# Optimization experiments

Hardware: AMD Instinct MI355X
Metric: run time of the kernel (lower is better)

## Reference

```python
import jax, jax.numpy as jnp
import numpy as np

D_MODEL = 256; D_FC = 1024; N_LEVELS = 4; N_HEADS = 8; N_POINTS = 4
D_HEAD = D_MODEL // N_HEADS
SPATIAL = np.array([[100, 100], [50, 50], [25, 25], [13, 13]], dtype=np.int64)
S_TOTAL = int((SPATIAL[:, 0] * SPATIAL[:, 1]).sum())  # 13294
BATCH = 2


def setup_inputs() -> dict:
    key = jax.random.key(0)
    ks = jax.random.split(key, 16)

    def lin(k, fi, fo):
        s = 1.0 / np.sqrt(fi)
        kw, kb = jax.random.split(k)
        W = jax.random.uniform(kw, (fi, fo), jnp.float32, -s, s)
        b = jax.random.uniform(kb, (fo,), jnp.float32, -s, s)
        return W, b

    W_off, b_off = lin(ks[0], D_MODEL, N_HEADS * N_LEVELS * N_POINTS * 2)
    W_attn, b_attn = lin(ks[1], D_MODEL, N_HEADS * N_LEVELS * N_POINTS)
    W_val, b_val = lin(ks[2], D_MODEL, D_MODEL)
    W_out, b_out = lin(ks[3], D_MODEL, D_MODEL)
    W1, b1 = lin(ks[4], D_MODEL, D_FC)
    W2, b2 = lin(ks[5], D_FC, D_MODEL)
    src = jax.random.normal(ks[6], (BATCH, S_TOTAL, D_MODEL), jnp.float32)
    pos = jax.random.normal(ks[7], (BATCH, S_TOTAL, D_MODEL), jnp.float32)
    reference_points = jax.random.uniform(ks[8], (BATCH, S_TOTAL, N_LEVELS, 2), jnp.float32)
    level_start_index = np.concatenate([[0], np.cumsum(SPATIAL[:, 0] * SPATIAL[:, 1])[:-1]]).astype(np.int64)
    return dict(src=src, pos=pos, reference_points=reference_points,
                spatial_shapes=SPATIAL, level_start_index=level_start_index,
                W_off=W_off, b_off=b_off, W_attn=W_attn, b_attn=b_attn,
                W_val=W_val, b_val=b_val, W_out=W_out, b_out=b_out,
                ln1_g=jnp.ones(D_MODEL, jnp.float32), ln1_b=jnp.zeros(D_MODEL, jnp.float32),
                W1=W1, b1=b1, W2=W2, b2=b2,
                ln2_g=jnp.ones(D_MODEL, jnp.float32), ln2_b=jnp.zeros(D_MODEL, jnp.float32))


def layernorm(x, g, b, eps=1e-5):
    mu = x.mean(-1, keepdims=True)
    var = ((x - mu) ** 2).mean(-1, keepdims=True)
    return (x - mu) * jax.lax.rsqrt(var + eps) * g + b


def ms_deform_attn(query, value_in, ref_pts, shapes,
                   W_off, b_off, W_attn, b_attn, W_val, b_val, W_out, b_out):
    N, Lq, _ = query.shape
    value = (value_in @ W_val + b_val).reshape(N, -1, N_HEADS, D_HEAD)
    off = (query @ W_off + b_off).reshape(N, Lq, N_HEADS, N_LEVELS, N_POINTS, 2)
    attn = (query @ W_attn + b_attn).reshape(N, Lq, N_HEADS, N_LEVELS * N_POINTS)
    attn = jax.nn.softmax(attn, -1).reshape(N, Lq, N_HEADS, N_LEVELS, N_POINTS)
    # offset normalizer is (W_l, H_l) per level
    norm = jnp.array([[w, h] for (h, w) in shapes], dtype=query.dtype)
    loc = ref_pts[:, :, None, :, None, :] + off / norm[None, None, None, :, None, :]
    out = jnp.zeros((N, Lq, N_HEADS, D_HEAD), query.dtype)
    start = 0
    for l, (H_, W_) in enumerate(shapes):
        v = value[:, start:start + H_ * W_].transpose(0, 2, 1, 3)  # [N, heads, HW, d]
        start += H_ * W_
        loc_l = loc[:, :, :, l]  # [N, Lq, heads, P, 2]
        # grid_sample(align_corners=False, padding_mode='zeros'): pixel = loc*size - 0.5
        px = loc_l[..., 0] * W_ - 0.5
        py = loc_l[..., 1] * H_ - 0.5
        x0 = jnp.floor(px); y0 = jnp.floor(py)
        wx = (px - x0)[..., None]; wy = (py - y0)[..., None]
        x0i = x0.astype(jnp.int32); y0i = y0.astype(jnp.int32)

        def samp(xi, yi):
            valid = (xi >= 0) & (xi < W_) & (yi >= 0) & (yi < H_)
            idx = jnp.clip(yi, 0, H_ - 1) * W_ + jnp.clip(xi, 0, W_ - 1)  # [N,Lq,heads,P]
            idx = idx.transpose(0, 2, 1, 3).reshape(N, N_HEADS, Lq * N_POINTS, 1)
            g = jnp.take_along_axis(v, idx, axis=2)  # [N,heads,Lq*P,d]
            g = g.reshape(N, N_HEADS, Lq, N_POINTS, D_HEAD).transpose(0, 2, 1, 3, 4)
            return g * valid[..., None]

        val = (samp(x0i, y0i) * (1 - wx) * (1 - wy)
               + samp(x0i + 1, y0i) * wx * (1 - wy)
               + samp(x0i, y0i + 1) * (1 - wx) * wy
               + samp(x0i + 1, y0i + 1) * wx * wy)  # [N,Lq,heads,P,d]
        out = out + (val * attn[:, :, :, l, :, None]).sum(3)
    return out.reshape(N, Lq, D_MODEL) @ W_out + b_out


def reference(src, pos, reference_points, spatial_shapes, level_start_index,
              W_off, b_off, W_attn, b_attn, W_val, b_val, W_out, b_out,
              ln1_g, ln1_b, W1, b1, W2, b2, ln2_g, ln2_b):
    shapes = [(int(spatial_shapes[l, 0]), int(spatial_shapes[l, 1])) for l in range(N_LEVELS)]
    q = src + pos
    attn_out = ms_deform_attn(q, src, reference_points, shapes,
                              W_off, b_off, W_attn, b_attn, W_val, b_val, W_out, b_out)
    x = layernorm(src + attn_out, ln1_g, ln1_b)  # dropout is identity in eval
    ffn = jax.nn.relu(x @ W1 + b1) @ W2 + b2
    return layernorm(x + ffn, ln2_g, ln2_b)
```

## Files before the change

kernel.cpp:

```cpp
#include <hip/hip_runtime.h>
#include <hip/hip_bf16.h>

#define DM 256
#define STOT 13294
#define MTOT (2 * STOT)

using bf16 = __hip_bfloat16;
typedef __attribute__((ext_vector_type(8))) short short8;
typedef __attribute__((ext_vector_type(4))) float floatx4;

#define GLDS16(g, l) __builtin_amdgcn_global_load_lds( \
    (const __attribute__((address_space(1))) void*)(g), \
    (__attribute__((address_space(3))) void*)(l), 16, 0, 0)

__device__ __forceinline__ float bu2f(unsigned u) { return __uint_as_float(u << 16); }
__device__ __forceinline__ unsigned short f2bu(float f) {
    union { bf16 h; unsigned short u; } c; c.h = __float2bfloat16(f); return c.u;
}

__global__ void detect_dtype(const unsigned* g1, int* flag) {
    if (threadIdx.x == 0 && blockIdx.x == 0)
        *flag = (g1[0] == 0x3F800000u) ? 1 : 0;
}

struct PW { const void* W[6]; const void* B[10]; };

__global__ void prep_weights(PW a, bf16* __restrict__ WT, float* __restrict__ bf,
                             const int* __restrict__ flag) {
    const long id = (long)blockIdx.x * 256 + threadIdx.x;
    const bool f32in = (*flag != 0);
    const int sz[6]  = {65536, 65536, 32768, 65536, 262144, 262144};
    const int Ns[6]  = {256, 256, 128, 256, 1024, 256};
    const int Ksh[6] = {8, 8, 8, 8, 8, 10};
    if (id < 753664) {
        long e = id; int j = 0;
        while (e >= sz[j]) { e -= sz[j]; ++j; }
        const int n = (int)(e >> Ksh[j]);
        const int k = (int)(e & ((1 << Ksh[j]) - 1));
        const size_t src = (size_t)k * Ns[j] + n;
        float v = f32in ? ((const float*)a.W[j])[src] : __bfloat162float(((const bf16*)a.W[j])[src]);
        WT[id] = __float2bfloat16(v);
    } else if (id < 753664 + 3200) {
        long e = id - 753664; int j = 0;
        const int bsz[10] = {256, 256, 128, 256, 1024, 256, 256, 256, 256, 256};
        while (e >= bsz[j]) { e -= bsz[j]; ++j; }
        float v = f32in ? ((const float*)a.B[j])[e] : __bfloat162float(((const bf16*)a.B[j])[e]);
        bf[id - 753664] = v;
    }
}

__global__ void prep_act(const void* __restrict__ src, const void* __restrict__ pos,
                         bf16* __restrict__ sbf, bf16* __restrict__ qbf,
                         const int* __restrict__ flag) {
    const long i = ((long)blockIdx.x * 256 + threadIdx.x) * 8;
    if (i >= (long)MTOT * DM) return;
    unsigned short ps[8], pq[8];
    if (*flag) {
        const float* s = (const float*)src + i;
        const float* p = (const float*)pos + i;
        float4 a0 = *(const float4*)s, a1 = *(const float4*)(s + 4);
        float4 b0 = *(const float4*)p, b1 = *(const float4*)(p + 4);
        const float av[8] = {a0.x, a0.y, a0.z, a0.w, a1.x, a1.y, a1.z, a1.w};
        const float bv[8] = {b0.x, b0.y, b0.z, b0.w, b1.x, b1.y, b1.z, b1.w};
#pragma unroll
        for (int j = 0; j < 8; ++j) { ps[j] = f2bu(av[j]); pq[j] = f2bu(av[j] + bv[j]); }
    } else {
        const unsigned short* s = (const unsigned short*)src + i;
        const unsigned short* p = (const unsigned short*)pos + i;
        uint4 a = *(const uint4*)s, b = *(const uint4*)p;
        const unsigned* ua = (const unsigned*)&a;
        const unsigned* ub = (const unsigned*)&b;
#pragma unroll
        for (int j = 0; j < 4; ++j) {
            float a0 = bu2f(ua[j] & 0xffffu), a1 = bu2f(ua[j] >> 16);
            float b0 = bu2f(ub[j] & 0xffffu), b1 = bu2f(ub[j] >> 16);
            ps[j * 2] = f2bu(a0); ps[j * 2 + 1] = f2bu(a1);
            pq[j * 2] = f2bu(a0 + b0); pq[j * 2 + 1] = f2bu(a1 + b1);
        }
    }
    *(uint4*)((unsigned short*)sbf + i) = *(const uint4*)ps;
    *(uint4*)((unsigned short*)qbf + i) = *(const uint4*)pq;
}

template<bool RELU>
__global__ __launch_bounds__(256, 4)
void gemm_bf16(const bf16* __restrict__ A0, const bf16* __restrict__ A1, int n_a0,
               const bf16* __restrict__ WT, const float* __restrict__ bias,
               bf16* __restrict__ C0, bf16* __restrict__ C1, bf16* __restrict__ C2,
               int M, int N, int K, int ldc0) {
    __shared__ __align__(16) bf16 sh[16384];
    const int t = threadIdx.x;
    const int wave = t >> 6, lane = t & 63;
    const int bm = blockIdx.y * 128, bn = blockIdx.x * 128;
    const bf16* __restrict__ A = (bn < n_a0) ? A0 : A1;
    const int wm = (wave >> 1) * 64, wn = (wave & 1) * 64;
    const int l15 = lane & 15, quad = lane >> 4;
    const int srow = lane >> 2, sko = (lane & 3) * 8;

    floatx4 acc[4][4];
#pragma unroll
    for (int i = 0; i < 4; ++i)
#pragma unroll
        for (int j = 0; j < 4; ++j) acc[i][j] = (floatx4)0.f;

    const int nb = K >> 5;
#pragma unroll
    for (int rh = 0; rh < 2; ++rh) {
        const int rbase = rh * 64 + wave * 16;
        const int gm = min(bm + rbase + srow, M - 1);
        GLDS16(A + (size_t)gm * K + sko, &sh[rbase * 32]);
        GLDS16(WT + (size_t)(bn + rbase + srow) * K + sko, &sh[8192 + rbase * 32]);
    }
    for (int i = 0; i < nb; ++i) {
        __syncthreads();
        if (i + 1 < nb) {
            const int k0 = (i + 1) << 5;
            const int bo = ((i + 1) & 1) * 4096;
#pragma unroll
            for (int rh = 0; rh < 2; ++rh) {
                const int rbase = rh * 64 + wave * 16;
                const int gm = min(bm + rbase + srow, M - 1);
                GLDS16(A + (size_t)gm * K + k0 + sko, &sh[bo + rbase * 32]);
                GLDS16(WT + (size_t)(bn + rbase + srow) * K + k0 + sko, &sh[8192 + bo + rbase * 32]);
            }
        }
        const int bo = (i & 1) * 4096;
        short8 af[4], bfr[4];
#pragma unroll
        for (int mi = 0; mi < 4; ++mi)
            af[mi] = *(const short8*)&sh[bo + (wm + mi * 16 + l15) * 32 + quad * 8];
#pragma unroll
        for (int nj = 0; nj < 4; ++nj)
            bfr[nj] = *(const short8*)&sh[8192 + bo + (wn + nj * 16 + l15) * 32 + quad * 8];
#pragma unroll
        for (int mi = 0; mi < 4; ++mi)
#pragma unroll
            for (int nj = 0; nj < 4; ++nj)
                acc[mi][nj] = __builtin_amdgcn_mfma_f32_16x16x32_bf16(bfr[nj], af[mi], acc[mi][nj], 0, 0, 0);
    }

    bf16* C = C0; int coloff = bn, ldc = ldc0;
    if (C1 != nullptr && bn >= 256) {
        if (C2 != nullptr && bn >= 512) { C = C2; coloff = bn - 512; ldc = 128; }
        else                            { C = C1; coloff = bn - 256; ldc = 256; }
    }
    float4 bv4[4];
#pragma unroll
    for (int nj = 0; nj < 4; ++nj)
        bv4[nj] = *(const float4*)&bias[bn + wn + nj * 16 + quad * 4];
#pragma unroll
    for (int mi = 0; mi < 4; ++mi) {
        const int gm = bm + wm + mi * 16 + l15;
        if (gm >= M) continue;
#pragma unroll
        for (int nj = 0; nj < 4; ++nj) {
            const float bb[4] = {bv4[nj].x, bv4[nj].y, bv4[nj].z, bv4[nj].w};
            unsigned short pk[4];
#pragma unroll
            for (int r = 0; r < 4; ++r) {
                float v = acc[mi][nj][r] + bb[r];
                if (RELU) v = fmaxf(v, 0.f);
                pk[r] = f2bu(v);
            }
            *(uint2*)&C[(size_t)gm * ldc + coloff + wn + nj * 16 + quad * 4] = *(const uint2*)pk;
        }
    }
}

__global__ void softmax16(bf16* __restrict__ a, int total) {
    const int i = blockIdx.x * 256 + threadIdx.x;
    if (i >= total) return;
    unsigned short* p = (unsigned short*)(a + (size_t)i * 16);
    uint4 r0 = *(const uint4*)p, r1 = *(const uint4*)(p + 8);
    float w[16];
    const unsigned* u0 = (const unsigned*)&r0;
    const unsigned* u1 = (const unsigned*)&r1;
#pragma unroll
    for (int j = 0; j < 4; ++j) {
        w[j * 2] = bu2f(u0[j] & 0xffffu); w[j * 2 + 1] = bu2f(u0[j] >> 16);
        w[8 + j * 2] = bu2f(u1[j] & 0xffffu); w[8 + j * 2 + 1] = bu2f(u1[j] >> 16);
    }
    float mx = -1e30f;
#pragma unroll
    for (int j = 0; j < 16; ++j) mx = fmaxf(mx, w[j]);
    float s = 0.f;
#pragma unroll
    for (int j = 0; j < 16; ++j) { w[j] = __expf(w[j] - mx); s += w[j]; }
    const float inv = 1.f / s;
    unsigned short pk[16];
#pragma unroll
    for (int j = 0; j < 16; ++j) pk[j] = f2bu(w[j] * inv);
    *(uint4*)p = *(const uint4*)pk;
    *(uint4*)(p + 8) = *(const uint4*)(pk + 8);
}

__device__ __forceinline__ void corner(const bf16* __restrict__ base, int xi, int yi,
                                       int W_, int H_, float wgt, float* acc) {
    const bool valid = (xi >= 0) & (xi < W_) & (yi >= 0) & (yi < H_);
    const int xc = min(max(xi, 0), W_ - 1);
    const int yc = min(max(yi, 0), H_ - 1);
    const ushort4 v = *(const ushort4*)(base + (size_t)(yc * W_ + xc) * DM);
    const float m = valid ? wgt : 0.f;
    acc[0] += m * bu2f(v.x); acc[1] += m * bu2f(v.y);
    acc[2] += m * bu2f(v.z); acc[3] += m * bu2f(v.w);
}

__global__ void deform_sample(const bf16* __restrict__ value, const bf16* __restrict__ off,
                              const bf16* __restrict__ attw, const void* __restrict__ refp,
                              bf16* __restrict__ out, const int* __restrict__ flag) {
    const int t = threadIdx.x;
    const int q = blockIdx.x * 4 + (t >> 6);
    const int ln = t & 63;
    const int h = ln >> 3, dg = ln & 7;
    const int b = (q >= STOT) ? 1 : 0;

    float w[16];
    {
        const unsigned short* wp = (const unsigned short*)(attw + (size_t)q * 128 + h * 16);
        uint4 r0 = *(const uint4*)wp, r1 = *(const uint4*)(wp + 8);
        const unsigned* u0 = (const unsigned*)&r0;
        const unsigned* u1 = (const unsigned*)&r1;
#pragma unroll
        for (int j = 0; j < 4; ++j) {
            w[j * 2] = bu2f(u0[j] & 0xffffu); w[j * 2 + 1] = bu2f(u0[j] >> 16);
            w[8 + j * 2] = bu2f(u1[j] & 0xffffu); w[8 + j * 2 + 1] = bu2f(u1[j] >> 16);
        }
    }
    float of[32];
    {
        const unsigned short* op = (const unsigned short*)(off + (size_t)q * 256 + h * 32);
#pragma unroll
        for (int c = 0; c < 4; ++c) {
            uint4 r = *(const uint4*)(op + c * 8);
            const unsigned* u = (const unsigned*)&r;
#pragma unroll
            for (int j = 0; j < 4; ++j) {
                of[c * 8 + j * 2] = bu2f(u[j] & 0xffffu);
                of[c * 8 + j * 2 + 1] = bu2f(u[j] >> 16);
            }
        }
    }
    float rxy[8];
    if (*flag) {
        const float* rp = (const float*)refp + (size_t)q * 8;
        float4 r0 = *(const float4*)rp, r1 = *(const float4*)(rp + 4);
        rxy[0] = r0.x; rxy[1] = r0.y; rxy[2] = r0.z; rxy[3] = r0.w;
        rxy[4] = r1.x; rxy[5] = r1.y; rxy[6] = r1.z; rxy[7] = r1.w;
    } else {
        const unsigned short* rp = (const unsigned short*)refp + (size_t)q * 8;
        uint4 r = *(const uint4*)rp;
        const unsigned* u = (const unsigned*)&r;
#pragma unroll
        for (int j = 0; j < 4; ++j) {
            rxy[j * 2] = bu2f(u[j] & 0xffffu); rxy[j * 2 + 1] = bu2f(u[j] >> 16);
        }
    }

    const int Hs4[4] = {100, 50, 25, 13};
    const int Ls[4] = {0, 10000, 12500, 13125};
    const bf16* vb = value + (size_t)(b * STOT) * DM + h * 32 + dg * 4;

    float acc[4] = {0.f, 0.f, 0.f, 0.f};
#pragma unroll
    for (int l = 0; l < 4; ++l) {
        const int W_ = Hs4[l], H_ = Hs4[l];
        const bf16* base = vb + (size_t)Ls[l] * DM;
        const float fw = (float)W_, fh = (float)H_;
#pragma unroll
        for (int p = 0; p < 4; ++p) {
            const float px = rxy[l * 2] * fw + of[(l * 4 + p) * 2] - 0.5f;
            const float py = rxy[l * 2 + 1] * fh + of[(l * 4 + p) * 2 + 1] - 0.5f;
            const float x0f = floorf(px), y0f = floorf(py);
            const float wx = px - x0f, wy = py - y0f;
            const int x0 = (int)x0f, y0 = (int)y0f;
            const float aw = w[l * 4 + p];
            const float ex = 1.f - wx, ey = 1.f - wy;
            corner(base, x0, y0, W_, H_, ex * ey * aw, acc);
            corner(base, x0 + 1, y0, W_, H_, wx * ey * aw, acc);
            corner(base, x0, y0 + 1, W_, H_, ex * wy * aw, acc);
            corner(base, x0 + 1, y0 + 1, W_, H_, wx * wy * aw, acc);
        }
    }
    unsigned short pk[4] = {f2bu(acc[0]), f2bu(acc[1]), f2bu(acc[2]), f2bu(acc[3])};
    *(ushort4*)((unsigned short*)out + (size_t)q * 256 + h * 32 + dg * 4) = *(const ushort4*)pk;
}

__global__ __launch_bounds__(512, 1)
void out_ln1(const bf16* __restrict__ vsamp, const bf16* __restrict__ srcbf,
             const bf16* __restrict__ WoT, const float* __restrict__ bo_f,
             const float* __restrict__ g1, const float* __restrict__ be1,
             bf16* __restrict__ vx, int M) {
    __shared__ __align__(16) bf16 Bs[8 * 4096];
    const int t = threadIdx.x, wave = t >> 6, lane = t & 63;
    const int l15 = lane & 15, quad = lane >> 4;
    const int srow = lane >> 2, sko = (lane & 3) * 8;
    const int bm = blockIdx.x * 128;
    const int mrow = bm + wave * 16 + l15;
    const int mc = min(mrow, M - 1);

    short8 af[8];
#pragma unroll
    for (int kk = 0; kk < 8; ++kk)
        af[kk] = *(const short8*)(vsamp + (size_t)mc * 256 + kk * 32 + quad * 8);

    floatx4 acc[16];
#pragma unroll
    for (int i = 0; i < 16; ++i) acc[i] = (floatx4)0.f;

    for (int nc = 0; nc < 2; ++nc) {
        __syncthreads();
#pragma unroll
        for (int rr = 0; rr < 8; ++rr)
            GLDS16(WoT + (size_t)(nc * 128 + rr * 16 + srow) * 256 + wave * 32 + sko,
                   &Bs[wave * 4096 + rr * 512]);
        __syncthreads();
#pragma unroll
        for (int kk = 0; kk < 8; ++kk)
#pragma unroll
            for (int nj = 0; nj < 8; ++nj) {
                short8 bfr = *(const short8*)&Bs[kk * 4096 + (nj * 16 + l15) * 32 + quad * 8];
                acc[nc * 8 + nj] = __builtin_amdgcn_mfma_f32_16x16x32_bf16(bfr, af[kk], acc[nc * 8 + nj], 0, 0, 0);
            }
    }

    float s = 0.f;
#pragma unroll
    for (int nj = 0; nj < 16; ++nj) {
        const int n = nj * 16 + quad * 4;
        const float4 bo = *(const float4*)&bo_f[n];
        const uint2 ru = *(const uint2*)(srcbf + (size_t)mc * 256 + n);
        const float rs[4] = {bu2f(ru.x & 0xffffu), bu2f(ru.x >> 16), bu2f(ru.y & 0xffffu), bu2f(ru.y >> 16)};
        const float bb[4] = {bo.x, bo.y, bo.z, bo.w};
#pragma unroll
        for (int r = 0; r < 4; ++r) { acc[nj][r] += bb[r] + rs[r]; s += acc[nj][r]; }
    }
    s += __shfl_xor(s, 16, 64); s += __shfl_xor(s, 32, 64);
    const float mean = s * (1.f / 256.f);
    float s2 = 0.f;
#pragma unroll
    for (int nj = 0; nj < 16; ++nj)
#pragma unroll
        for (int r = 0; r < 4; ++r) { const float c = acc[nj][r] - mean; s2 += c * c; }
    s2 += __shfl_xor(s2, 16, 64); s2 += __shfl_xor(s2, 32, 64);
    const float rstd = rsqrtf(s2 * (1.f / 256.f) + 1e-5f);
    if (mrow < M) {
#pragma unroll
        for (int nj = 0; nj < 16; ++nj) {
            const int n = nj * 16 + quad * 4;
            const float4 g = *(const float4*)&g1[n];
            const float4 b = *(const float4*)&be1[n];
            const float gg[4] = {g.x, g.y, g.z, g.w}, bb[4] = {b.x, b.y, b.z, b.w};
            unsigned short pk[4];
#pragma unroll
            for (int r = 0; r < 4; ++r) pk[r] = f2bu((acc[nj][r] - mean) * rstd * gg[r] + bb[r]);
            *(uint2*)&vx[(size_t)mrow * 256 + n] = *(const uint2*)pk;
        }
    }
}

__global__ __launch_bounds__(512, 1)
void ffn_ln2(const bf16* __restrict__ vx, const bf16* __restrict__ W1T, const bf16* __restrict__ W2T,
             const float* __restrict__ b1f, const float* __restrict__ b2f,
             const float* __restrict__ g2, const float* __restrict__ be2,
             void* __restrict__ outp, const int* __restrict__ flag, int M) {
    __shared__ __align__(16) bf16 Bs1[8 * 4096];
    __shared__ __align__(16) bf16 Bs2[4 * 4096];
    __shared__ __align__(16) bf16 Hs[128 * 136];
    const int t = threadIdx.x, wave = t >> 6, lane = t & 63;
    const int l15 = lane & 15, quad = lane >> 4;
    const int srow = lane >> 2, sko = (lane & 3) * 8;
    const int bm = blockIdx.x * 128;
    const int mrow = bm + wave * 16 + l15;
    const int mc = min(mrow, M - 1);

    short8 af[8];
#pragma unroll
    for (int kk = 0; kk < 8; ++kk)
        af[kk] = *(const short8*)(vx + (size_t)mc * 256 + kk * 32 + quad * 8);

    floatx4 acc2[16];
#pragma unroll
    for (int i = 0; i < 16; ++i) acc2[i] = (floatx4)0.f;

    const int kp = wave >> 1, rh = wave & 1;

    for (int ch = 0; ch < 8; ++ch) {
        __syncthreads();
#pragma unroll
        for (int rr = 0; rr < 8; ++rr)
            GLDS16(W1T + (size_t)(ch * 128 + rr * 16 + srow) * 256 + wave * 32 + sko,
                   &Bs1[wave * 4096 + rr * 512]);
#pragma unroll
        for (int rr = 0; rr < 4; ++rr)
            GLDS16(W2T + (size_t)(rh * 64 + rr * 16 + srow) * 1024 + ch * 128 + kp * 32 + sko,
                   &Bs2[kp * 4096 + (rh * 64 + rr * 16) * 32]);
        __syncthreads();

        floatx4 acc1[8];
#pragma unroll
        for (int i = 0; i < 8; ++i) acc1[i] = (floatx4)0.f;
#pragma unroll
        for (int kk = 0; kk < 8; ++kk)
#pragma unroll
            for (int nj = 0; nj < 8; ++nj) {
                short8 bfr = *(const short8*)&Bs1[kk * 4096 + (nj * 16 + l15) * 32 + quad * 8];
                acc1[nj] = __builtin_amdgcn_mfma_f32_16x16x32_bf16(bfr, af[kk], acc1[nj], 0, 0, 0);
            }
#pragma unroll
        for (int nj = 0; nj < 8; ++nj) {
            const float4 bb = *(const float4*)&b1f[ch * 128 + nj * 16 + quad * 4];
            const float bv[4] = {bb.x, bb.y, bb.z, bb.w};
            unsigned short pk[4];
#pragma unroll
            for (int r = 0; r < 4; ++r) pk[r] = f2bu(fmaxf(acc1[nj][r] + bv[r], 0.f));
            *(uint2*)&Hs[(wave * 16 + l15) * 136 + nj * 16 + quad * 4] = *(const uint2*)pk;
        }
        short8 ah[4];
#pragma unroll
        for (int kq = 0; kq < 4; ++kq)
            ah[kq] = *(const short8*)&Hs[(wave * 16 + l15) * 136 + kq * 32 + quad * 8];
#pragma unroll
        for (int kq = 0; kq < 4; ++kq)
#pragma unroll
            for (int nj = 0; nj < 8; ++nj) {
                short8 bfr = *(const short8*)&Bs2[kq * 4096 + (nj * 16 + l15) * 32 + quad * 8];
                acc2[nj] = __builtin_amdgcn_mfma_f32_16x16x32_bf16(bfr, ah[kq], acc2[nj], 0, 0, 0);
            }
        __syncthreads();
#pragma unroll
        for (int rr = 0; rr < 4; ++rr)
            GLDS16(W2T + (size_t)(128 + rh * 64 + rr * 16 + srow) * 1024 + ch * 128 + kp * 32 + sko,
                   &Bs2[kp * 4096 + (rh * 64 + rr * 16) * 32]);
        __syncthreads();
#pragma unroll
        for (int kq = 0; kq < 4; ++kq)
#pragma unroll
            for (int nj = 0; nj < 8; ++nj) {
                short8 bfr = *(const short8*)&Bs2[kq * 4096 + (nj * 16 + l15) * 32 + quad * 8];
                acc2[8 + nj] = __builtin_amdgcn_mfma_f32_16x16x32_bf16(bfr, ah[kq], acc2[8 + nj], 0, 0, 0);
            }
    }

    float s = 0.f;
#pragma unroll
    for (int nj = 0; nj < 16; ++nj) {
        const int n = nj * 16 + quad * 4;
        const float4 bo = *(const float4*)&b2f[n];
        const uint2 ru = *(const uint2*)(vx + (size_t)mc * 256 + n);
        const float rs[4] = {bu2f(ru.x & 0xffffu), bu2f(ru.x >> 16), bu2f(ru.y & 0xffffu), bu2f(ru.y >> 16)};
        const float bb[4] = {bo.x, bo.y, bo.z, bo.w};
#pragma unroll
        for (int r = 0; r < 4; ++r) { acc2[nj][r] += bb[r] + rs[r]; s += acc2[nj][r]; }
    }
    s += __shfl_xor(s, 16, 64); s += __shfl_xor(s, 32, 64);
    const float mean = s * (1.f / 256.f);
    float s2 = 0.f;
#pragma unroll
    for (int nj = 0; nj < 16; ++nj)
#pragma unroll
        for (int r = 0; r < 4; ++r) { const float c = acc2[nj][r] - mean; s2 += c * c; }
    s2 += __shfl_xor(s2, 16, 64); s2 += __shfl_xor(s2, 32, 64);
    const float rstd = rsqrtf(s2 * (1.f / 256.f) + 1e-5f);
    if (mrow < M) {
        const bool f32o = (*flag != 0);
#pragma unroll
        for (int nj = 0; nj < 16; ++nj) {
            const int n = nj * 16 + quad * 4;
            const float4 g = *(const float4*)&g2[n];
            const float4 b = *(const float4*)&be2[n];
            const float gg[4] = {g.x, g.y, g.z, g.w}, bb[4] = {b.x, b.y, b.z, b.w};
            float y[4];
#pragma unroll
            for (int r = 0; r < 4; ++r) y[r] = (acc2[nj][r] - mean) * rstd * gg[r] + bb[r];
            if (f32o) {
                float4 o = {y[0], y[1], y[2], y[3]};
                *(float4*)((float*)outp + (size_t)mrow * 256 + n) = o;
            } else {
                unsigned short pk[4] = {f2bu(y[0]), f2bu(y[1]), f2bu(y[2]), f2bu(y[3])};
                *(uint2*)((bf16*)outp + (size_t)mrow * 256 + n) = *(const uint2*)pk;
            }
        }
    }
}

extern "C" void kernel_launch(void* const* d_in, const int* in_sizes, int n_in,
                              void* d_out, int out_size, void* d_ws, size_t ws_size,
                              hipStream_t stream) {
    const void* src   = d_in[0];
    const void* pos   = d_in[1];
    const void* refp  = d_in[2];
    const void* W_off = d_in[5];
    const void* b_off = d_in[6];
    const void* W_att = d_in[7];
    const void* b_att = d_in[8];
    const void* W_val = d_in[9];
    const void* b_val = d_in[10];
    const void* W_out = d_in[11];
    const void* b_out = d_in[12];
    const void* ln1g  = d_in[13];
    const void* ln1b  = d_in[14];
    const void* W1    = d_in[15];
    const void* b1    = d_in[16];
    const void* W2    = d_in[17];
    const void* b2    = d_in[18];
    const void* ln2g  = d_in[19];
    const void* ln2b  = d_in[20];

    const size_t M = MTOT;
    bf16* src_bf = (bf16*)d_ws;
    bf16* q_bf   = src_bf + M * 256;
    bf16* v_val  = src_bf + M * 512;
    bf16* v_off  = src_bf + M * 768;
    bf16* v_attn = src_bf + M * 1024;
    bf16* v_samp = src_bf + M * 1152;
    bf16* v_x    = src_bf + M * 1408;
    bf16* WT     = src_bf + M * 1664;
    float* biasf = (float*)(WT + 753664);
    int* flag    = (int*)(biasf + 3200);

    dim3 blk(256);
    const int mg = (MTOT + 127) / 128;

    detect_dtype<<<1, 64, 0, stream>>>((const unsigned*)ln1g, flag);

    PW pw;
    pw.W[0] = W_val; pw.W[1] = W_off; pw.W[2] = W_att; pw.W[3] = W_out; pw.W[4] = W1; pw.W[5] = W2;
    pw.B[0] = b_val; pw.B[1] = b_off; pw.B[2] = b_att; pw.B[3] = b_out; pw.B[4] = b1; pw.B[5] = b2;
    pw.B[6] = ln1g;  pw.B[7] = ln1b;  pw.B[8] = ln2g;  pw.B[9] = ln2b;
    prep_weights<<<(753664 + 3200 + 255) / 256, blk, 0, stream>>>(pw, WT, biasf, flag);
    prep_act<<<(int)((M * 256 / 8 + 255) / 256), blk, 0, stream>>>(src, pos, src_bf, q_bf, flag);

    gemm_bf16<false><<<dim3(5, mg), blk, 0, stream>>>(src_bf, q_bf, 256, WT, biasf,
                                                      v_val, v_off, v_attn, MTOT, 640, 256, 256);
    softmax16<<<(MTOT * 8 + 255) / 256, blk, 0, stream>>>(v_attn, MTOT * 8);
    deform_sample<<<MTOT / 4, blk, 0, stream>>>(v_val, v_off, v_attn, refp, v_samp, flag);
    out_ln1<<<mg, dim3(512), 0, stream>>>(v_samp, src_bf, WT + 163840, biasf + 640,
                                          biasf + 2176, biasf + 2432, v_x, MTOT);
    ffn_ln2<<<mg, dim3(512), 0, stream>>>(v_x, WT + 229376, WT + 491520,
                                          biasf + 896, biasf + 1920,
                                          biasf + 2688, biasf + 2944,
                                          d_out, flag, MTOT);
}
```

Before: 322.0 us.

## Retile fused FFN+LN2 kernel to 64-row blocks with 2x2 wave split

The fused FFN/LayerNorm2 kernel moves from 128-row blocks of 512 threads (8 waves, each owning 16 rows and all 256 output columns) to 64-row blocks of 256 threads. Each wave now owns 32 rows and half of the hidden/output columns, and the two column halves exchange row sums through shared memory for the LayerNorm. This halves shared memory per block and lowers per-wave register pressure so two blocks can share a CU, and each loaded weight fragment is reused across two row tiles. In exchange there are more __syncthreads in the K loops and a cross-wave reduction. The variance is now computed as E[x²]−mean² in one pass, which is slightly less numerically robust.

```diff
diff --git a/kernel.cpp b/kernel.cpp
--- a/kernel.cpp
+++ b/kernel.cpp
@@ -358,126 +358,154 @@
     }
 }
 
-__global__ __launch_bounds__(512, 1)
+__global__ __launch_bounds__(256, 2)
 void ffn_ln2(const bf16* __restrict__ vx, const bf16* __restrict__ W1T, const bf16* __restrict__ W2T,
              const float* __restrict__ b1f, const float* __restrict__ b2f,
              const float* __restrict__ g2, const float* __restrict__ be2,
              void* __restrict__ outp, const int* __restrict__ flag, int M) {
-    __shared__ __align__(16) bf16 Bs1[8 * 4096];
-    __shared__ __align__(16) bf16 Bs2[4 * 4096];
-    __shared__ __align__(16) bf16 Hs[128 * 136];
-    const int t = threadIdx.x, wave = t >> 6, lane = t & 63;
+    __shared__ __align__(16) bf16 Bs1[16384];
+    __shared__ __align__(16) bf16 Bs2[8192];
+    __shared__ __align__(16) bf16 Hs[64 * 136];
+    __shared__ float2 red[128];
+    const int t = threadIdx.x, wv = t >> 6, lane = t & 63;
     const int l15 = lane & 15, quad = lane >> 4;
+    const int g = wv & 1, nh = wv >> 1;
     const int srow = lane >> 2, sko = (lane & 3) * 8;
-    const int bm = blockIdx.x * 128;
-    const int mrow = bm + wave * 16 + l15;
-    const int mc = min(mrow, M - 1);
-
-    short8 af[8];
-#pragma unroll
-    for (int kk = 0; kk < 8; ++kk)
-        af[kk] = *(const short8*)(vx + (size_t)mc * 256 + kk * 32 + quad * 8);
-
-    floatx4 acc2[16];
-#pragma unroll
-    for (int i = 0; i < 16; ++i) acc2[i] = (floatx4)0.f;
-
-    const int kp = wave >> 1, rh = wave & 1;
+    const int bm = blockIdx.x * 64;
+
+    int mrow[2], mc[2];
+#pragma unroll
+    for (int mi = 0; mi < 2; ++mi) {
+        mrow[mi] = bm + g * 32 + mi * 16 + l15;
+        mc[mi] = min(mrow[mi], M - 1);
+    }
+    short8 af[2][8];
+#pragma unroll
+    for (int mi = 0; mi < 2; ++mi)
+#pragma unroll
+        for (int kk = 0; kk < 8; ++kk)
+            af[mi][kk] = *(const short8*)(vx + (size_t)mc[mi] * 256 + kk * 32 + quad * 8);
+
+    floatx4 acc2[2][8];
+#pragma unroll
+    for (int mi = 0; mi < 2; ++mi)
+#pragma unroll
+        for (int nj = 0; nj < 8; ++nj) acc2[mi][nj] = (floatx4)0.f;
 
     for (int ch = 0; ch < 8; ++ch) {
-        __syncthreads();
-#pragma unroll
-        for (int rr = 0; rr < 8; ++rr)
-            GLDS16(W1T + (size_t)(ch * 128 + rr * 16 + srow) * 256 + wave * 32 + sko,
-                   &Bs1[wave * 4096 + rr * 512]);
-#pragma unroll
-        for (int rr = 0; rr < 4; ++rr)
-            GLDS16(W2T + (size_t)(rh * 64 + rr * 16 + srow) * 1024 + ch * 128 + kp * 32 + sko,
-                   &Bs2[kp * 4096 + (rh * 64 + rr * 16) * 32]);
-        __syncthreads();
-
-        floatx4 acc1[8];
-#pragma unroll
-        for (int i = 0; i < 8; ++i) acc1[i] = (floatx4)0.f;
-#pragma unroll
-        for (int kk = 0; kk < 8; ++kk)
+        floatx4 acc1[2][4];
+#pragma unroll
+        for (int mi = 0; mi < 2; ++mi)
+#pragma unroll
+            for (int nj = 0; nj < 4; ++nj) acc1[mi][nj] = (floatx4)0.f;
+#pragma unroll
+        for (int ks = 0; ks < 2; ++ks) {
+            __syncthreads();
+#pragma unroll
+            for (int j = 0; j < 8; ++j)
+                GLDS16(W1T + (size_t)(ch * 128 + j * 16 + srow) * 256 + ks * 128 + wv * 32 + sko,
+                       &Bs1[wv * 4096 + j * 512]);
+            __syncthreads();
+#pragma unroll
+            for (int kk = 0; kk < 4; ++kk) {
+                short8 bfr[4];
+#pragma unroll
+                for (int nj = 0; nj < 4; ++nj)
+                    bfr[nj] = *(const short8*)&Bs1[kk * 4096 + (nh * 64 + nj * 16 + l15) * 32 + quad * 8];
+#pragma unroll
+                for (int mi = 0; mi < 2; ++mi)
+#pragma unroll
+                    for (int nj = 0; nj < 4; ++nj)
+                        acc1[mi][nj] = __builtin_amdgcn_mfma_f32_16x16x32_bf16(bfr[nj], af[mi][ks * 4 + kk], acc1[mi][nj], 0, 0, 0);
+            }
+        }
+#pragma unroll
+        for (int mi = 0; mi < 2; ++mi)
+#pragma unroll
+            for (int nj = 0; nj < 4; ++nj) {
+                const int kl = nh * 64 + nj * 16 + quad * 4;
+                const float4 bb = *(const float4*)&b1f[ch * 128 + kl];
+                const float bv[4] = {bb.x, bb.y, bb.z, bb.w};
+                unsigned short pk[4];
+#pragma unroll
+                for (int r = 0; r < 4; ++r) pk[r] = f2bu(fmaxf(acc1[mi][nj][r] + bv[r], 0.f));
+                *(uint2*)&Hs[(g * 32 + mi * 16 + l15) * 136 + kl] = *(const uint2*)pk;
+            }
+#pragma unroll
+        for (int p = 0; p < 4; ++p) {
+            __syncthreads();
+#pragma unroll
+            for (int j = 0; j < 4; ++j)
+                GLDS16(W2T + (size_t)(wv * 64 + j * 16 + srow) * 1024 + ch * 128 + p * 32 + sko,
+                       &Bs2[(wv * 64 + j * 16) * 32]);
+            __syncthreads();
+            short8 ah[2];
+#pragma unroll
+            for (int mi = 0; mi < 2; ++mi)
+                ah[mi] = *(const short8*)&Hs[(g * 32 + mi * 16 + l15) * 136 + p * 32 + quad * 8];
 #pragma unroll
             for (int nj = 0; nj < 8; ++nj) {
-                short8 bfr = *(const short8*)&Bs1[kk * 4096 + (nj * 16 + l15) * 32 + quad * 8];
-                acc1[nj] = __builtin_amdgcn_mfma_f32_16x16x32_bf16(bfr, af[kk], acc1[nj], 0, 0, 0);
-            }
+                short8 bfr = *(const short8*)&Bs2[(nh * 128 + nj * 16 + l15) * 32 + quad * 8];
+#pragma unroll
+                for (int mi = 0; mi < 2; ++mi)
+                    acc2[mi][nj] = __builtin_amdgcn_mfma_f32_16x16x32_bf16(bfr, ah[mi], acc2[mi][nj], 0, 0, 0);
+            }
+        }
+    }
+
+    float sm[2] = {0.f, 0.f}, sq[2] = {0.f, 0.f};
+#pragma unroll
+    for (int mi = 0; mi < 2; ++mi)
 #pragma unroll
         for (int nj = 0; nj < 8; ++nj) {
-            const float4 bb = *(const float4*)&b1f[ch * 128 + nj * 16 + quad * 4];
-            const float bv[4] = {bb.x, bb.y, bb.z, bb.w};
-            unsigned short pk[4];
-#pragma unroll
-            for (int r = 0; r < 4; ++r) pk[r] = f2bu(fmaxf(acc1[nj][r] + bv[r], 0.f));
-            *(uint2*)&Hs[(wave * 16 + l15) * 136 + nj * 16 + quad * 4] = *(const uint2*)pk;
-        }
-        short8 ah[4];
-#pragma unroll
-        for (int kq = 0; kq < 4; ++kq)
-            ah[kq] = *(const short8*)&Hs[(wave * 16 + l15) * 136 + kq * 32 + quad * 8];
-#pragma unroll
-        for (int kq = 0; kq < 4; ++kq)
+            const int n = nh * 128 + nj * 16 + quad * 4;
+            const float4 bo = *(const float4*)&b2f[n];
+            const uint2 ru = *(const uint2*)(vx + (size_t)mc[mi] * 256 + n);
+            const float rs[4] = {bu2f(ru.x & 0xffffu), bu2f(ru.x >> 16), bu2f(ru.y & 0xffffu), bu2f(ru.y >> 16)};
+            const float bb[4] = {bo.x, bo.y, bo.z, bo.w};
+#pragma unroll
+            for (int r = 0; r < 4; ++r) {
+                const float v = acc2[mi][nj][r] + bb[r] + rs[r];
+                acc2[mi][nj][r] = v; sm[mi] += v; sq[mi] += v * v;
+            }
+        }
+#pragma unroll
+    for (int mi = 0; mi < 2; ++mi) {
+        sm[mi] += __shfl_xor(sm[mi], 16, 64); sm[mi] += __shfl_xor(sm[mi], 32, 64);
+        sq[mi] += __shfl_xor(sq[mi], 16, 64); sq[mi] += __shfl_xor(sq[mi], 32, 64);
+    }
+    __syncthreads();
+    if (quad == 0) {
+#pragma unroll
+        for (int mi = 0; mi < 2; ++mi)
+            red[((nh * 2 + g) * 2 + mi) * 16 + l15] = make_float2(sm[mi], sq[mi]);
+    }
+    __syncthreads();
+    const bool f32o = (*flag != 0);
+#pragma unroll
+    for (int mi = 0; mi < 2; ++mi) {
+        const float2 o = red[(((1 - nh) * 2 + g) * 2 + mi) * 16 + l15];
+        const float ts = sm[mi] + o.x, tq = sq[mi] + o.y;
+        const float mean = ts * (1.f / 256.f);
+        const float var = tq * (1.f / 256.f) - mean * mean;
+        const float rstd = rsqrtf(var + 1e-5f);
+        if (mrow[mi] < M) {
 #pragma unroll
             for (int nj = 0; nj < 8; ++nj) {
-                short8 bfr = *(const short8*)&Bs2[kq * 4096 + (nj * 16 + l15) * 32 + quad * 8];
-                acc2[nj] = __builtin_amdgcn_mfma_f32_16x16x32_bf16(bfr, ah[kq], acc2[nj], 0, 0, 0);
-            }
-        __syncthreads();
-#pragma unroll
-        for (int rr = 0; rr < 4; ++rr)
-            GLDS16(W2T + (size_t)(128 + rh * 64 + rr * 16 + srow) * 1024 + ch * 128 + kp * 32 + sko,
-                   &Bs2[kp * 4096 + (rh * 64 + rr * 16) * 32]);
-        __syncthreads();
-#pragma unroll
-        for (int kq = 0; kq < 4; ++kq)
-#pragma unroll
-            for (int nj = 0; nj < 8; ++nj) {
-                short8 bfr = *(const short8*)&Bs2[kq * 4096 + (nj * 16 + l15) * 32 + quad * 8];
-                acc2[8 + nj] = __builtin_amdgcn_mfma_f32_16x16x32_bf16(bfr, ah[kq], acc2[8 + nj], 0, 0, 0);
-            }
-    }
-
-    float s = 0.f;
-#pragma unroll
-    for (int nj = 0; nj < 16; ++nj) {
-        const int n = nj * 16 + quad * 4;
-        const float4 bo = *(const float4*)&b2f[n];
-        const uint2 ru = *(const uint2*)(vx + (size_t)mc * 256 + n);
-        const float rs[4] = {bu2f(ru.x & 0xffffu), bu2f(ru.x >> 16), bu2f(ru.y & 0xffffu), bu2f(ru.y >> 16)};
-        const float bb[4] = {bo.x, bo.y, bo.z, bo.w};
-#pragma unroll
-        for (int r = 0; r < 4; ++r) { acc2[nj][r] += bb[r] + rs[r]; s += acc2[nj][r]; }
-    }
-    s += __shfl_xor(s, 16, 64); s += __shfl_xor(s, 32, 64);
-    const float mean = s * (1.f / 256.f);
-    float s2 = 0.f;
-#pragma unroll
-    for (int nj = 0; nj < 16; ++nj)
-#pragma unroll
-        for (int r = 0; r < 4; ++r) { const float c = acc2[nj][r] - mean; s2 += c * c; }
-    s2 += __shfl_xor(s2, 16, 64); s2 += __shfl_xor(s2, 32, 64);
-    const float rstd = rsqrtf(s2 * (1.f / 256.f) + 1e-5f);
-    if (mrow < M) {
-        const bool f32o = (*flag != 0);
-#pragma unroll
-        for (int nj = 0; nj < 16; ++nj) {
-            const int n = nj * 16 + quad * 4;
-            const float4 g = *(const float4*)&g2[n];
-            const float4 b = *(const float4*)&be2[n];
-            const float gg[4] = {g.x, g.y, g.z, g.w}, bb[4] = {b.x, b.y, b.z, b.w};
-            float y[4];
-#pragma unroll
-            for (int r = 0; r < 4; ++r) y[r] = (acc2[nj][r] - mean) * rstd * gg[r] + bb[r];
-            if (f32o) {
-                float4 o = {y[0], y[1], y[2], y[3]};
-                *(float4*)((float*)outp + (size_t)mrow * 256 + n) = o;
-            } else {
-                unsigned short pk[4] = {f2bu(y[0]), f2bu(y[1]), f2bu(y[2]), f2bu(y[3])};
-                *(uint2*)((bf16*)outp + (size_t)mrow * 256 + n) = *(const uint2*)pk;
+                const int n = nh * 128 + nj * 16 + quad * 4;
+                const float4 gv = *(const float4*)&g2[n];
+                const float4 bv = *(const float4*)&be2[n];
+                const float gg[4] = {gv.x, gv.y, gv.z, gv.w}, bb[4] = {bv.x, bv.y, bv.z, bv.w};
+                float y[4];
+#pragma unroll
+                for (int r = 0; r < 4; ++r) y[r] = (acc2[mi][nj][r] - mean) * rstd * gg[r] + bb[r];
+                if (f32o) {
+                    float4 ov = {y[0], y[1], y[2], y[3]};
+                    *(float4*)((float*)outp + (size_t)mrow[mi] * 256 + n) = ov;
+                } else {
+                    unsigned short pk[4] = {f2bu(y[0]), f2bu(y[1]), f2bu(y[2]), f2bu(y[3])};
+                    *(uint2*)((bf16*)outp + (size_t)mrow[mi] * 256 + n) = *(const uint2*)pk;
+                }
             }
         }
     }
@@ -536,8 +564,8 @@
     deform_sample<<<MTOT / 4, blk, 0, stream>>>(v_val, v_off, v_attn, refp, v_samp, flag);
     out_ln1<<<mg, dim3(512), 0, stream>>>(v_samp, src_bf, WT + 163840, biasf + 640,
                                           biasf + 2176, biasf + 2432, v_x, MTOT);
-    ffn_ln2<<<mg, dim3(512), 0, stream>>>(v_x, WT + 229376, WT + 491520,
-                                          biasf + 896, biasf + 1920,
-                                          biasf + 2688, biasf + 2944,
-                                          d_out, flag, MTOT);
-}
+    ffn_ln2<<<(MTOT + 63) / 64, blk, 0, stream>>>(v_x, WT + 229376, WT + 491520,
+                                                  biasf + 896, biasf + 1920,
+                                                  biasf + 2688, biasf + 2944,
+                                                  d_out, flag, MTOT);
+}
```

Result: faster. 310.0 us (-3.7%).
